# Kernel tuning notes

Measured on AMD Instinct MI355X. Metric: run time of the kernel, lower is better.

Reference implementation:

```python
import jax, jax.numpy as jnp
import numpy as np

BETA = 0.25

def setup_inputs() -> dict:
    key = jax.random.key(0)
    k1, k2 = jax.random.split(key)
    z = jax.random.normal(k1, (4096, 64, 64), dtype=jnp.float32)
    codebooks = jax.random.normal(k2, (64, 256, 64), dtype=jnp.float32)
    return {"z": z, "codebooks": codebooks}

def reference(z, codebooks):
    # z: (B, M, d); codebooks: (M, K, d)
    B, M, d = z.shape
    # squared distances (B, M, K) via ||z||^2 - 2 z.c + ||c||^2 (avoids (B,M,K,d) blowup)
    z2 = jnp.sum(z * z, axis=-1)                      # (B, M)
    c2 = jnp.sum(codebooks * codebooks, axis=-1)      # (M, K)
    zc = jnp.einsum('bmd,mkd->bmk', z, codebooks)     # (B, M, K)
    distances = z2[:, :, None] - 2.0 * zc + c2[None]  # (B, M, K)
    encoding_indices = jnp.argmin(distances, axis=-1) # (B, M) int
    # per-subspace codebook gather: codebooks[m, idx[b, m], :]
    quantized_raw = codebooks[jnp.arange(M)[None, :], encoding_indices]  # (B, M, d)
    # straight-through estimator
    quantized = z + jax.lax.stop_gradient(quantized_raw - z)
    q_loss = (BETA * jnp.mean((jax.lax.stop_gradient(quantized) - z) ** 2)
              + jnp.mean((quantized - jax.lax.stop_gradient(z)) ** 2))
    return quantized, encoding_indices, q_loss
```

## Files before the change

kernel.cpp:

```cpp
#include <hip/hip_runtime.h>

#define IDX_BASE 16777216UL
#define LOSS_IDX 17039360UL
#define EPS2 0.02f

typedef float4 f4;
typedef _Float16 half8 __attribute__((ext_vector_type(8)));
typedef float f32x4 __attribute__((ext_vector_type(4)));

__device__ __forceinline__ void gload_lds16(const float* g, float* s) {
    __builtin_amdgcn_global_load_lds(
        (const __attribute__((address_space(1))) unsigned int*)g,
        (__attribute__((address_space(3))) unsigned int*)s, 16, 0, 0);
}

__global__ __launch_bounds__(256) void pq_c2(const float* __restrict__ cb,
                                             float* __restrict__ c2) {
    int m = blockIdx.x, k = threadIdx.x;
    const f4* row = reinterpret_cast<const f4*>(cb + ((size_t)m * 256 + k) * 64);
    float s0 = 0.f, s1 = 0.f;
    #pragma unroll
    for (int i = 0; i < 16; i += 2) {
        f4 a = row[i], b = row[i + 1];
        s0 = fmaf(a.x,a.x,s0); s0 = fmaf(a.y,a.y,s0); s0 = fmaf(a.z,a.z,s0); s0 = fmaf(a.w,a.w,s0);
        s1 = fmaf(b.x,b.x,s1); s1 = fmaf(b.y,b.y,s1); s1 = fmaf(b.z,b.z,s1); s1 = fmaf(b.w,b.w,s1);
    }
    c2[m * 256 + k] = s0 + s1;
}

__global__ __launch_bounds__(256, 4) void pq_main(
    const float* __restrict__ z, const float* __restrict__ cb,
    const float* __restrict__ c2ws,
    float* __restrict__ out, float* __restrict__ partial)
{
    __shared__ f4    sZ4[128 * 16];
    __shared__ float sM1[4 * 128];
    __shared__ float sM2[4 * 128];
    __shared__ int   sK [4 * 128];
    __shared__ int   sBest[128];
    __shared__ float sW[4];

    const int tid = threadIdx.x, bx = blockIdx.x;
    const int m = bx >> 5, chunk = bx & 31;
    const int w = tid >> 6, lane = tid & 63;
    const int lh = lane >> 4, l15 = lane & 15;

    const float* __restrict__ cbm = cb + (size_t)m * (256 * 64);
    const f4* cb4m = reinterpret_cast<const f4*>(cbm);

    #pragma unroll
    for (int i = 0; i < 8; ++i) {
        int unit = i * 256 + w * 64 + lane;
        int row = unit >> 4, c4 = unit & 15;
        int c4p = c4 ^ (row & 7);
        const float* src = z + ((size_t)(chunk * 128 + row) * 64 + m) * 64 + c4p * 4;
        gload_lds16(src, (float*)&sZ4[i * 256 + w * 64]);
    }

    half8 ah[4][2], al[4][2];
    #pragma unroll
    for (int t = 0; t < 4; ++t) {
        int code = (w * 4 + t) * 16 + l15;
        const float* crow = cbm + code * 64 + lh * 8;
        #pragma unroll
        for (int s = 0; s < 2; ++s) {
            f4 a = *reinterpret_cast<const f4*>(crow + s * 32);
            f4 b = *reinterpret_cast<const f4*>(crow + s * 32 + 4);
            float v[8] = {a.x, a.y, a.z, a.w, b.x, b.y, b.z, b.w};
            #pragma unroll
            for (int e = 0; e < 8; ++e) {
                _Float16 h = (_Float16)v[e];
                ah[t][s][e] = h;
                al[t][s][e] = (_Float16)(v[e] - (float)h);
            }
        }
    }
    f32x4 c2i[4];
    #pragma unroll
    for (int t = 0; t < 4; ++t)
        #pragma unroll
        for (int r = 0; r < 4; ++r)
            c2i[t][r] = -0.5f * c2ws[m * 256 + w * 64 + t * 16 + lh * 4 + r];

    __syncthreads();

    #pragma unroll 1
    for (int rt = 0; rt < 8; ++rt) {
        const int row = rt * 16 + l15;
        const int swz = row & 7;
        const f4* zr = &sZ4[row * 16];
        const int c0 = lh << 1;
        f4 a0 = zr[(c0)     ^ swz];
        f4 a1 = zr[(c0 + 1) ^ swz];
        f4 a2 = zr[(c0 + 8) ^ swz];
        f4 a3 = zr[(c0 + 9) ^ swz];
        half8 bh0, bl0, bh1, bl1;
        {
            float v0[8] = {a0.x, a0.y, a0.z, a0.w, a1.x, a1.y, a1.z, a1.w};
            float v1[8] = {a2.x, a2.y, a2.z, a2.w, a3.x, a3.y, a3.z, a3.w};
            #pragma unroll
            for (int e = 0; e < 8; ++e) {
                _Float16 h0 = (_Float16)v0[e];
                bh0[e] = h0; bl0[e] = (_Float16)(v0[e] - (float)h0);
                _Float16 h1 = (_Float16)v1[e];
                bh1[e] = h1; bl1[e] = (_Float16)(v1[e] - (float)h1);
            }
        }
        float m1 = -1e30f, m2 = -1e30f; int k16 = 0;
        #pragma unroll
        for (int t = 0; t < 4; ++t) {
            f32x4 acc = c2i[t];
            acc = __builtin_amdgcn_mfma_f32_16x16x32_f16(ah[t][0], bh0, acc, 0, 0, 0);
            acc = __builtin_amdgcn_mfma_f32_16x16x32_f16(ah[t][1], bh1, acc, 0, 0, 0);
            acc = __builtin_amdgcn_mfma_f32_16x16x32_f16(ah[t][0], bl0, acc, 0, 0, 0);
            acc = __builtin_amdgcn_mfma_f32_16x16x32_f16(ah[t][1], bl1, acc, 0, 0, 0);
            acc = __builtin_amdgcn_mfma_f32_16x16x32_f16(al[t][0], bh0, acc, 0, 0, 0);
            acc = __builtin_amdgcn_mfma_f32_16x16x32_f16(al[t][1], bh1, acc, 0, 0, 0);
            #pragma unroll
            for (int r = 0; r < 4; ++r) {
                float v = acc[r];
                m2 = fmaxf(m2, fminf(v, m1));
                bool gt = v > m1;
                m1  = gt ? v : m1;
                k16 = gt ? (t * 16 + r) : k16;
            }
        }
        int kw = k16 + lh * 4;
        #pragma unroll
        for (int off = 16; off <= 32; off <<= 1) {
            float om1 = __shfl_xor(m1, off, 64);
            float om2 = __shfl_xor(m2, off, 64);
            int   okw = __shfl_xor(kw, off, 64);
            m2 = fmaxf(fmaxf(m2, om2), fminf(m1, om1));
            bool better = (om1 > m1) || (om1 == m1 && okw < kw);
            m1 = better ? om1 : m1;
            kw = better ? okw : kw;
        }
        if (lane < 16) {
            int r2 = rt * 16 + lane;
            sM1[w * 128 + r2] = m1;
            sM2[w * 128 + r2] = m2;
            sK [w * 128 + r2] = kw;
        }
    }
    __syncthreads();

    if (tid < 128) {
        float M1 = -1e30f, M2 = -1e30f; int K1 = 0;
        #pragma unroll
        for (int w2 = 0; w2 < 4; ++w2) {
            float v1 = sM1[w2 * 128 + tid];
            float v2 = sM2[w2 * 128 + tid];
            int   kk = w2 * 64 + sK[w2 * 128 + tid];
            M2 = fmaxf(fmaxf(M2, v2), fminf(M1, v1));
            bool better = v1 > M1;
            M1 = better ? v1 : M1;
            K1 = better ? kk : K1;
        }
        sBest[tid] = (M1 - M2 < EPS2) ? -1 : K1;
    }
    __syncthreads();

    for (int row = w; row < 128; row += 4) {
        if (sBest[row] >= 0) continue;
        int swz = row & 7;
        float bs = -1e30f; int bk = 0;
        #pragma unroll 1
        for (int j = 0; j < 4; ++j) {
            int k = j * 64 + lane;
            float s = -0.5f * c2ws[m * 256 + k];
            #pragma unroll
            for (int d4 = 0; d4 < 16; ++d4) {
                f4 c  = cb4m[k * 16 + d4];
                f4 zz = sZ4[row * 16 + (d4 ^ swz)];
                s = fmaf(zz.x, c.x, s); s = fmaf(zz.y, c.y, s);
                s = fmaf(zz.z, c.z, s); s = fmaf(zz.w, c.w, s);
            }
            if (s > bs) { bs = s; bk = k; }
        }
        #pragma unroll
        for (int off = 1; off < 64; off <<= 1) {
            float ov = __shfl_xor(bs, off, 64);
            int   ok = __shfl_xor(bk, off, 64);
            if (ov > bs || (ov == bs && ok < bk)) { bs = ov; bk = ok; }
        }
        if (lane == 0) sBest[row] = bk;
    }
    __syncthreads();

    float lsum = 0.f;
    {
        int row = tid >> 1, h = tid & 1;
        int k = sBest[row];
        int b = chunk * 128 + row;
        int swz = row & 7;
        const f4* q4 = cb4m + (size_t)k * 16 + h * 8;
        f4*       o4 = reinterpret_cast<f4*>(out + ((size_t)b * 64 + m) * 64) + h * 8;
        float l0 = 0.f, l1 = 0.f;
        #pragma unroll
        for (int c = 0; c < 8; ++c) {
            f4 qv = q4[c];
            f4 zv = sZ4[row * 16 + (((h << 3) + c) ^ swz)];
            o4[c] = qv;
            float d0 = qv.x - zv.x, d1 = qv.y - zv.y, d2 = qv.z - zv.z, d3 = qv.w - zv.w;
            l0 = fmaf(d0, d0, l0); l1 = fmaf(d1, d1, l1);
            l0 = fmaf(d2, d2, l0); l1 = fmaf(d3, d3, l1);
        }
        lsum = l0 + l1;
    }
    if (tid < 128)
        out[IDX_BASE + (size_t)(chunk * 128 + tid) * 64 + m] = (float)sBest[tid];
    #pragma unroll
    for (int off = 1; off < 64; off <<= 1) lsum += __shfl_xor(lsum, off, 64);
    if (lane == 0) sW[w] = lsum;
    __syncthreads();
    if (tid == 0) partial[bx] = (sW[0] + sW[1]) + (sW[2] + sW[3]);
}

__global__ __launch_bounds__(256) void pq_loss(const float* __restrict__ partial,
                                               float* __restrict__ out)
{
    __shared__ float sW[4];
    float s = 0.f;
    #pragma unroll
    for (int i = 0; i < 8; ++i) s += partial[threadIdx.x + i * 256];
    #pragma unroll
    for (int off = 1; off < 64; off <<= 1) s += __shfl_xor(s, off, 64);
    if ((threadIdx.x & 63) == 0) sW[threadIdx.x >> 6] = s;
    __syncthreads();
    if (threadIdx.x == 0)
        out[LOSS_IDX] = ((sW[0] + sW[1]) + (sW[2] + sW[3])) * (1.25f / 16777216.0f);
}

extern "C" void kernel_launch(void* const* d_in, const int* in_sizes, int n_in,
                              void* d_out, int out_size, void* d_ws, size_t ws_size,
                              hipStream_t stream) {
    const float* zp  = (const float*)d_in[0];
    const float* cbp = (const float*)d_in[1];
    float* outp = (float*)d_out;
    float* c2ws = (float*)d_ws;
    float* part = (float*)d_ws + 64 * 256;

    pq_c2  <<<dim3(64),   dim3(256), 0, stream>>>(cbp, c2ws);
    pq_main<<<dim3(2048), dim3(256), 0, stream>>>(zp, cbp, c2ws, outp, part);
    pq_loss<<<dim3(1),    dim3(256), 0, stream>>>(part, outp);
}
```

Baseline: 93.04 us.

## Make main kernel persistent over four 64-row chunks with double-buffered z staging

Each block now handles four 64-row chunks of one subspace instead of a single 128-row chunk, so the grid halves to 1024 blocks. The next chunk's z tile is loaded into LDS asynchronously while the current one is processed, and the codebook fragments in fp16 hi/lo form are reused across all four chunks. This amortizes the per-block codebook conversion and hides z load latency. The cost is more barriers per block and fewer blocks to fill the GPU, and smaller chunks may expose the serial fallback path more often.

```diff
diff --git a/kernel.cpp b/kernel.cpp
--- a/kernel.cpp
+++ b/kernel.cpp
@@ -3,6 +3,8 @@
 #define IDX_BASE 16777216UL
 #define LOSS_IDX 17039360UL
 #define EPS2 0.02f
+#define NCHUNK 4
+#define CROWS 64
 
 typedef float4 f4;
 typedef _Float16 half8 __attribute__((ext_vector_type(8)));
@@ -33,29 +35,33 @@
     const float* __restrict__ c2ws,
     float* __restrict__ out, float* __restrict__ partial)
 {
-    __shared__ f4    sZ4[128 * 16];
-    __shared__ float sM1[4 * 128];
-    __shared__ float sM2[4 * 128];
-    __shared__ int   sK [4 * 128];
-    __shared__ int   sBest[128];
+    __shared__ f4    sZ4[2][CROWS * 16];
+    __shared__ float sM1[4 * CROWS];
+    __shared__ float sM2[4 * CROWS];
+    __shared__ int   sK [4 * CROWS];
+    __shared__ int   sBest[CROWS];
     __shared__ float sW[4];
 
     const int tid = threadIdx.x, bx = blockIdx.x;
-    const int m = bx >> 5, chunk = bx & 31;
+    const int m = bx >> 4, g = bx & 15;
     const int w = tid >> 6, lane = tid & 63;
     const int lh = lane >> 4, l15 = lane & 15;
+    const int cbase = g * NCHUNK;
 
     const float* __restrict__ cbm = cb + (size_t)m * (256 * 64);
     const f4* cb4m = reinterpret_cast<const f4*>(cbm);
 
-    #pragma unroll
-    for (int i = 0; i < 8; ++i) {
-        int unit = i * 256 + w * 64 + lane;
-        int row = unit >> 4, c4 = unit & 15;
-        int c4p = c4 ^ (row & 7);
-        const float* src = z + ((size_t)(chunk * 128 + row) * 64 + m) * 64 + c4p * 4;
-        gload_lds16(src, (float*)&sZ4[i * 256 + w * 64]);
-    }
+    auto stage = [&](int c, int bb) {
+        #pragma unroll
+        for (int i = 0; i < 4; ++i) {
+            int unit = i * 256 + w * 64 + lane;
+            int row = unit >> 4, c4 = unit & 15;
+            int c4p = c4 ^ (row & 7);
+            const float* src = z + ((size_t)(c * 64 + row) * 64 + m) * 64 + c4p * 4;
+            gload_lds16(src, (float*)&sZ4[bb][i * 256 + w * 64]);
+        }
+    };
+    stage(cbase, 0);
 
     half8 ah[4][2], al[4][2];
     #pragma unroll
@@ -82,137 +88,145 @@
         for (int r = 0; r < 4; ++r)
             c2i[t][r] = -0.5f * c2ws[m * 256 + w * 64 + t * 16 + lh * 4 + r];
 
-    __syncthreads();
+    float lacc = 0.f;
 
     #pragma unroll 1
-    for (int rt = 0; rt < 8; ++rt) {
-        const int row = rt * 16 + l15;
-        const int swz = row & 7;
-        const f4* zr = &sZ4[row * 16];
-        const int c0 = lh << 1;
-        f4 a0 = zr[(c0)     ^ swz];
-        f4 a1 = zr[(c0 + 1) ^ swz];
-        f4 a2 = zr[(c0 + 8) ^ swz];
-        f4 a3 = zr[(c0 + 9) ^ swz];
-        half8 bh0, bl0, bh1, bl1;
+    for (int cc = 0; cc < NCHUNK; ++cc) {
+        const int cur = cc & 1, nxt = cur ^ 1;
+        const int c = cbase + cc;
+        __syncthreads();
+        if (cc + 1 < NCHUNK) stage(c + 1, nxt);
+        const f4* zt = sZ4[cur];
+
+        #pragma unroll 1
+        for (int rt = 0; rt < 4; ++rt) {
+            const int row = rt * 16 + l15;
+            const int swz = row & 7;
+            const f4* zr = &zt[row * 16];
+            const int c0 = lh << 1;
+            f4 a0 = zr[(c0)     ^ swz];
+            f4 a1 = zr[(c0 + 1) ^ swz];
+            f4 a2 = zr[(c0 + 8) ^ swz];
+            f4 a3 = zr[(c0 + 9) ^ swz];
+            half8 bh0, bl0, bh1, bl1;
+            {
+                float v0[8] = {a0.x, a0.y, a0.z, a0.w, a1.x, a1.y, a1.z, a1.w};
+                float v1[8] = {a2.x, a2.y, a2.z, a2.w, a3.x, a3.y, a3.z, a3.w};
+                #pragma unroll
+                for (int e = 0; e < 8; ++e) {
+                    _Float16 h0 = (_Float16)v0[e];
+                    bh0[e] = h0; bl0[e] = (_Float16)(v0[e] - (float)h0);
+                    _Float16 h1 = (_Float16)v1[e];
+                    bh1[e] = h1; bl1[e] = (_Float16)(v1[e] - (float)h1);
+                }
+            }
+            float m1 = -1e30f, m2 = -1e30f; int k16 = 0;
+            #pragma unroll
+            for (int t = 0; t < 4; ++t) {
+                f32x4 acc = c2i[t];
+                acc = __builtin_amdgcn_mfma_f32_16x16x32_f16(ah[t][0], bh0, acc, 0, 0, 0);
+                acc = __builtin_amdgcn_mfma_f32_16x16x32_f16(ah[t][1], bh1, acc, 0, 0, 0);
+                acc = __builtin_amdgcn_mfma_f32_16x16x32_f16(ah[t][0], bl0, acc, 0, 0, 0);
+                acc = __builtin_amdgcn_mfma_f32_16x16x32_f16(ah[t][1], bl1, acc, 0, 0, 0);
+                acc = __builtin_amdgcn_mfma_f32_16x16x32_f16(al[t][0], bh0, acc, 0, 0, 0);
+                acc = __builtin_amdgcn_mfma_f32_16x16x32_f16(al[t][1], bh1, acc, 0, 0, 0);
+                #pragma unroll
+                for (int r = 0; r < 4; ++r) {
+                    float v = acc[r];
+                    m2 = fmaxf(m2, fminf(v, m1));
+                    bool gt = v > m1;
+                    m1  = gt ? v : m1;
+                    k16 = gt ? (t * 16 + r) : k16;
+                }
+            }
+            int kw = k16 + lh * 4;
+            #pragma unroll
+            for (int off = 16; off <= 32; off <<= 1) {
+                float om1 = __shfl_xor(m1, off, 64);
+                float om2 = __shfl_xor(m2, off, 64);
+                int   okw = __shfl_xor(kw, off, 64);
+                m2 = fmaxf(fmaxf(m2, om2), fminf(m1, om1));
+                bool better = (om1 > m1) || (om1 == m1 && okw < kw);
+                m1 = better ? om1 : m1;
+                kw = better ? okw : kw;
+            }
+            if (lane < 16) {
+                int r2 = rt * 16 + lane;
+                sM1[w * CROWS + r2] = m1;
+                sM2[w * CROWS + r2] = m2;
+                sK [w * CROWS + r2] = kw;
+            }
+        }
+        __syncthreads();
+
+        if (tid < CROWS) {
+            float M1 = -1e30f, M2 = -1e30f; int K1 = 0;
+            #pragma unroll
+            for (int w2 = 0; w2 < 4; ++w2) {
+                float v1 = sM1[w2 * CROWS + tid];
+                float v2 = sM2[w2 * CROWS + tid];
+                int   kk = w2 * 64 + sK[w2 * CROWS + tid];
+                M2 = fmaxf(fmaxf(M2, v2), fminf(M1, v1));
+                bool better = v1 > M1;
+                M1 = better ? v1 : M1;
+                K1 = better ? kk : K1;
+            }
+            sBest[tid] = (M1 - M2 < EPS2) ? -1 : K1;
+        }
+        __syncthreads();
+
+        for (int row = w; row < CROWS; row += 4) {
+            if (sBest[row] >= 0) continue;
+            int swz = row & 7;
+            float bs = -1e30f; int bk = 0;
+            #pragma unroll 1
+            for (int j = 0; j < 4; ++j) {
+                int k = j * 64 + lane;
+                float s = -0.5f * c2ws[m * 256 + k];
+                #pragma unroll
+                for (int d4 = 0; d4 < 16; ++d4) {
+                    f4 cvv = cb4m[k * 16 + d4];
+                    f4 zz  = zt[row * 16 + (d4 ^ swz)];
+                    s = fmaf(zz.x, cvv.x, s); s = fmaf(zz.y, cvv.y, s);
+                    s = fmaf(zz.z, cvv.z, s); s = fmaf(zz.w, cvv.w, s);
+                }
+                if (s > bs) { bs = s; bk = k; }
+            }
+            #pragma unroll
+            for (int off = 1; off < 64; off <<= 1) {
+                float ov = __shfl_xor(bs, off, 64);
+                int   ok = __shfl_xor(bk, off, 64);
+                if (ov > bs || (ov == bs && ok < bk)) { bs = ov; bk = ok; }
+            }
+            if (lane == 0) sBest[row] = bk;
+        }
+        __syncthreads();
+
         {
-            float v0[8] = {a0.x, a0.y, a0.z, a0.w, a1.x, a1.y, a1.z, a1.w};
-            float v1[8] = {a2.x, a2.y, a2.z, a2.w, a3.x, a3.y, a3.z, a3.w};
-            #pragma unroll
-            for (int e = 0; e < 8; ++e) {
-                _Float16 h0 = (_Float16)v0[e];
-                bh0[e] = h0; bl0[e] = (_Float16)(v0[e] - (float)h0);
-                _Float16 h1 = (_Float16)v1[e];
-                bh1[e] = h1; bl1[e] = (_Float16)(v1[e] - (float)h1);
-            }
-        }
-        float m1 = -1e30f, m2 = -1e30f; int k16 = 0;
-        #pragma unroll
-        for (int t = 0; t < 4; ++t) {
-            f32x4 acc = c2i[t];
-            acc = __builtin_amdgcn_mfma_f32_16x16x32_f16(ah[t][0], bh0, acc, 0, 0, 0);
-            acc = __builtin_amdgcn_mfma_f32_16x16x32_f16(ah[t][1], bh1, acc, 0, 0, 0);
-            acc = __builtin_amdgcn_mfma_f32_16x16x32_f16(ah[t][0], bl0, acc, 0, 0, 0);
-            acc = __builtin_amdgcn_mfma_f32_16x16x32_f16(ah[t][1], bl1, acc, 0, 0, 0);
-            acc = __builtin_amdgcn_mfma_f32_16x16x32_f16(al[t][0], bh0, acc, 0, 0, 0);
-            acc = __builtin_amdgcn_mfma_f32_16x16x32_f16(al[t][1], bh1, acc, 0, 0, 0);
-            #pragma unroll
-            for (int r = 0; r < 4; ++r) {
-                float v = acc[r];
-                m2 = fmaxf(m2, fminf(v, m1));
-                bool gt = v > m1;
-                m1  = gt ? v : m1;
-                k16 = gt ? (t * 16 + r) : k16;
-            }
-        }
-        int kw = k16 + lh * 4;
-        #pragma unroll
-        for (int off = 16; off <= 32; off <<= 1) {
-            float om1 = __shfl_xor(m1, off, 64);
-            float om2 = __shfl_xor(m2, off, 64);
-            int   okw = __shfl_xor(kw, off, 64);
-            m2 = fmaxf(fmaxf(m2, om2), fminf(m1, om1));
-            bool better = (om1 > m1) || (om1 == m1 && okw < kw);
-            m1 = better ? om1 : m1;
-            kw = better ? okw : kw;
-        }
-        if (lane < 16) {
-            int r2 = rt * 16 + lane;
-            sM1[w * 128 + r2] = m1;
-            sM2[w * 128 + r2] = m2;
-            sK [w * 128 + r2] = kw;
-        }
+            int row = tid >> 2, quad = tid & 3;
+            int k = sBest[row];
+            int b = c * 64 + row;
+            int swz = row & 7;
+            const f4* q4 = cb4m + (size_t)k * 16 + quad * 4;
+            f4*       o4 = reinterpret_cast<f4*>(out + ((size_t)b * 64 + m) * 64) + quad * 4;
+            #pragma unroll
+            for (int e = 0; e < 4; ++e) {
+                f4 qv = q4[e];
+                f4 zv = zt[row * 16 + ((quad * 4 + e) ^ swz)];
+                o4[e] = qv;
+                float d0 = qv.x - zv.x, d1 = qv.y - zv.y;
+                float d2 = qv.z - zv.z, d3 = qv.w - zv.w;
+                lacc = fmaf(d0, d0, lacc); lacc = fmaf(d1, d1, lacc);
+                lacc = fmaf(d2, d2, lacc); lacc = fmaf(d3, d3, lacc);
+            }
+        }
+        if (tid < CROWS)
+            out[IDX_BASE + (size_t)(c * 64 + tid) * 64 + m] = (float)sBest[tid];
     }
-    __syncthreads();
-
-    if (tid < 128) {
-        float M1 = -1e30f, M2 = -1e30f; int K1 = 0;
-        #pragma unroll
-        for (int w2 = 0; w2 < 4; ++w2) {
-            float v1 = sM1[w2 * 128 + tid];
-            float v2 = sM2[w2 * 128 + tid];
-            int   kk = w2 * 64 + sK[w2 * 128 + tid];
-            M2 = fmaxf(fmaxf(M2, v2), fminf(M1, v1));
-            bool better = v1 > M1;
-            M1 = better ? v1 : M1;
-            K1 = better ? kk : K1;
-        }
-        sBest[tid] = (M1 - M2 < EPS2) ? -1 : K1;
-    }
-    __syncthreads();
-
-    for (int row = w; row < 128; row += 4) {
-        if (sBest[row] >= 0) continue;
-        int swz = row & 7;
-        float bs = -1e30f; int bk = 0;
-        #pragma unroll 1
-        for (int j = 0; j < 4; ++j) {
-            int k = j * 64 + lane;
-            float s = -0.5f * c2ws[m * 256 + k];
-            #pragma unroll
-            for (int d4 = 0; d4 < 16; ++d4) {
-                f4 c  = cb4m[k * 16 + d4];
-                f4 zz = sZ4[row * 16 + (d4 ^ swz)];
-                s = fmaf(zz.x, c.x, s); s = fmaf(zz.y, c.y, s);
-                s = fmaf(zz.z, c.z, s); s = fmaf(zz.w, c.w, s);
-            }
-            if (s > bs) { bs = s; bk = k; }
-        }
-        #pragma unroll
-        for (int off = 1; off < 64; off <<= 1) {
-            float ov = __shfl_xor(bs, off, 64);
-            int   ok = __shfl_xor(bk, off, 64);
-            if (ov > bs || (ov == bs && ok < bk)) { bs = ov; bk = ok; }
-        }
-        if (lane == 0) sBest[row] = bk;
-    }
-    __syncthreads();
-
-    float lsum = 0.f;
-    {
-        int row = tid >> 1, h = tid & 1;
-        int k = sBest[row];
-        int b = chunk * 128 + row;
-        int swz = row & 7;
-        const f4* q4 = cb4m + (size_t)k * 16 + h * 8;
-        f4*       o4 = reinterpret_cast<f4*>(out + ((size_t)b * 64 + m) * 64) + h * 8;
-        float l0 = 0.f, l1 = 0.f;
-        #pragma unroll
-        for (int c = 0; c < 8; ++c) {
-            f4 qv = q4[c];
-            f4 zv = sZ4[row * 16 + (((h << 3) + c) ^ swz)];
-            o4[c] = qv;
-            float d0 = qv.x - zv.x, d1 = qv.y - zv.y, d2 = qv.z - zv.z, d3 = qv.w - zv.w;
-            l0 = fmaf(d0, d0, l0); l1 = fmaf(d1, d1, l1);
-            l0 = fmaf(d2, d2, l0); l1 = fmaf(d3, d3, l1);
-        }
-        lsum = l0 + l1;
-    }
-    if (tid < 128)
-        out[IDX_BASE + (size_t)(chunk * 128 + tid) * 64 + m] = (float)sBest[tid];
-    #pragma unroll
-    for (int off = 1; off < 64; off <<= 1) lsum += __shfl_xor(lsum, off, 64);
-    if (lane == 0) sW[w] = lsum;
+
+    #pragma unroll
+    for (int off = 1; off < 64; off <<= 1) lacc += __shfl_xor(lacc, off, 64);
+    if (lane == 0) sW[w] = lacc;
     __syncthreads();
     if (tid == 0) partial[bx] = (sW[0] + sW[1]) + (sW[2] + sW[3]);
 }
@@ -221,9 +235,8 @@
                                                float* __restrict__ out)
 {
     __shared__ float sW[4];
-    float s = 0.f;
-    #pragma unroll
-    for (int i = 0; i < 8; ++i) s += partial[threadIdx.x + i * 256];
+    float s = (partial[threadIdx.x]       + partial[threadIdx.x + 256])
+            + (partial[threadIdx.x + 512] + partial[threadIdx.x + 768]);
     #pragma unroll
     for (int off = 1; off < 64; off <<= 1) s += __shfl_xor(s, off, 64);
     if ((threadIdx.x & 63) == 0) sW[threadIdx.x >> 6] = s;
@@ -242,6 +255,6 @@
     float* part = (float*)d_ws + 64 * 256;
 
     pq_c2  <<<dim3(64),   dim3(256), 0, stream>>>(cbp, c2ws);
-    pq_main<<<dim3(2048), dim3(256), 0, stream>>>(zp, cbp, c2ws, outp, part);
+    pq_main<<<dim3(1024), dim3(256), 0, stream>>>(zp, cbp, c2ws, outp, part);
     pq_loss<<<dim3(1),    dim3(256), 0, stream>>>(part, outp);
 }
```

Result: slower. 150.9 us (+62.2%).

## Swap MFMA roles: keep z fragments in registers, stream precomputed codebook fragments

Applied to the files above, without the earlier changes.

A new pre-kernel converts each subspace codebook into split fp16 hi/lo MFMA fragments once and stores them in workspace. Each wave in the main kernel now owns 32 z rows held as register fragments and loops over all 16 codebook tiles read from that buffer. This removes the LDS staging of z, the cross-wave argmin merge and most block barriers. In exchange the codebook fragments are re-read from global/L2 by every wave, and the exact-recheck path reads z straight from global memory.

```diff
diff --git a/kernel.cpp b/kernel.cpp
--- a/kernel.cpp
+++ b/kernel.cpp
@@ -7,12 +7,6 @@
 typedef float4 f4;
 typedef _Float16 half8 __attribute__((ext_vector_type(8)));
 typedef float f32x4 __attribute__((ext_vector_type(4)));
-
-__device__ __forceinline__ void gload_lds16(const float* g, float* s) {
-    __builtin_amdgcn_global_load_lds(
-        (const __attribute__((address_space(1))) unsigned int*)g,
-        (__attribute__((address_space(3))) unsigned int*)s, 16, 0, 0);
-}
 
 __global__ __launch_bounds__(256) void pq_c2(const float* __restrict__ cb,
                                              float* __restrict__ c2) {
@@ -28,193 +22,168 @@
     c2[m * 256 + k] = s0 + s1;
 }
 
-__global__ __launch_bounds__(256, 4) void pq_main(
-    const float* __restrict__ z, const float* __restrict__ cb,
-    const float* __restrict__ c2ws,
-    float* __restrict__ out, float* __restrict__ partial)
-{
-    __shared__ f4    sZ4[128 * 16];
-    __shared__ float sM1[4 * 128];
-    __shared__ float sM2[4 * 128];
-    __shared__ int   sK [4 * 128];
-    __shared__ int   sBest[128];
-    __shared__ float sW[4];
-
-    const int tid = threadIdx.x, bx = blockIdx.x;
-    const int m = bx >> 5, chunk = bx & 31;
-    const int w = tid >> 6, lane = tid & 63;
-    const int lh = lane >> 4, l15 = lane & 15;
-
-    const float* __restrict__ cbm = cb + (size_t)m * (256 * 64);
-    const f4* cb4m = reinterpret_cast<const f4*>(cbm);
-
-    #pragma unroll
-    for (int i = 0; i < 8; ++i) {
-        int unit = i * 256 + w * 64 + lane;
-        int row = unit >> 4, c4 = unit & 15;
-        int c4p = c4 ^ (row & 7);
-        const float* src = z + ((size_t)(chunk * 128 + row) * 64 + m) * 64 + c4p * 4;
-        gload_lds16(src, (float*)&sZ4[i * 256 + w * 64]);
-    }
-
-    half8 ah[4][2], al[4][2];
-    #pragma unroll
-    for (int t = 0; t < 4; ++t) {
-        int code = (w * 4 + t) * 16 + l15;
+__global__ __launch_bounds__(256) void pq_frag(const float* __restrict__ cb,
+                                               half8* __restrict__ fragbuf) {
+    int m = blockIdx.x, tid = threadIdx.x;
+    int w = tid >> 6, lane = tid & 63, lh = lane >> 4, l15 = lane & 15;
+    const float* cbm = cb + (size_t)m * (256 * 64);
+    half8* fbm = fragbuf + (size_t)m * (16 * 4 * 64);
+    #pragma unroll
+    for (int ti = 0; ti < 4; ++ti) {
+        int tile = w * 4 + ti;
+        int code = tile * 16 + l15;
         const float* crow = cbm + code * 64 + lh * 8;
         #pragma unroll
         for (int s = 0; s < 2; ++s) {
             f4 a = *reinterpret_cast<const f4*>(crow + s * 32);
             f4 b = *reinterpret_cast<const f4*>(crow + s * 32 + 4);
             float v[8] = {a.x, a.y, a.z, a.w, b.x, b.y, b.z, b.w};
+            half8 hi, lo;
             #pragma unroll
             for (int e = 0; e < 8; ++e) {
                 _Float16 h = (_Float16)v[e];
-                ah[t][s][e] = h;
-                al[t][s][e] = (_Float16)(v[e] - (float)h);
-            }
-        }
-    }
-    f32x4 c2i[4];
-    #pragma unroll
-    for (int t = 0; t < 4; ++t)
-        #pragma unroll
-        for (int r = 0; r < 4; ++r)
-            c2i[t][r] = -0.5f * c2ws[m * 256 + w * 64 + t * 16 + lh * 4 + r];
-
-    __syncthreads();
-
-    #pragma unroll 1
-    for (int rt = 0; rt < 8; ++rt) {
-        const int row = rt * 16 + l15;
-        const int swz = row & 7;
-        const f4* zr = &sZ4[row * 16];
-        const int c0 = lh << 1;
-        f4 a0 = zr[(c0)     ^ swz];
-        f4 a1 = zr[(c0 + 1) ^ swz];
-        f4 a2 = zr[(c0 + 8) ^ swz];
-        f4 a3 = zr[(c0 + 9) ^ swz];
-        half8 bh0, bl0, bh1, bl1;
-        {
-            float v0[8] = {a0.x, a0.y, a0.z, a0.w, a1.x, a1.y, a1.z, a1.w};
-            float v1[8] = {a2.x, a2.y, a2.z, a2.w, a3.x, a3.y, a3.z, a3.w};
-            #pragma unroll
-            for (int e = 0; e < 8; ++e) {
-                _Float16 h0 = (_Float16)v0[e];
-                bh0[e] = h0; bl0[e] = (_Float16)(v0[e] - (float)h0);
-                _Float16 h1 = (_Float16)v1[e];
-                bh1[e] = h1; bl1[e] = (_Float16)(v1[e] - (float)h1);
-            }
-        }
-        float m1 = -1e30f, m2 = -1e30f; int k16 = 0;
-        #pragma unroll
-        for (int t = 0; t < 4; ++t) {
-            f32x4 acc = c2i[t];
-            acc = __builtin_amdgcn_mfma_f32_16x16x32_f16(ah[t][0], bh0, acc, 0, 0, 0);
-            acc = __builtin_amdgcn_mfma_f32_16x16x32_f16(ah[t][1], bh1, acc, 0, 0, 0);
-            acc = __builtin_amdgcn_mfma_f32_16x16x32_f16(ah[t][0], bl0, acc, 0, 0, 0);
-            acc = __builtin_amdgcn_mfma_f32_16x16x32_f16(ah[t][1], bl1, acc, 0, 0, 0);
-            acc = __builtin_amdgcn_mfma_f32_16x16x32_f16(al[t][0], bh0, acc, 0, 0, 0);
-            acc = __builtin_amdgcn_mfma_f32_16x16x32_f16(al[t][1], bh1, acc, 0, 0, 0);
+                hi[e] = h; lo[e] = (_Float16)(v[e] - (float)h);
+            }
+            fbm[(tile * 4 + s * 2 + 0) * 64 + lane] = hi;
+            fbm[(tile * 4 + s * 2 + 1) * 64 + lane] = lo;
+        }
+    }
+}
+
+__global__ __launch_bounds__(256, 4) void pq_main(
+    const float* __restrict__ z, const float* __restrict__ cb,
+    const float* __restrict__ c2ws, const half8* __restrict__ fragbuf,
+    float* __restrict__ out, float* __restrict__ partial)
+{
+    const int tid = threadIdx.x, bx = blockIdx.x;
+    const int m = bx >> 5;
+    const int w = tid >> 6, lane = tid & 63;
+    const int lh = lane >> 4, l15 = lane & 15;
+    const int rowbase = (bx & 31) * 128 + w * 32;
+
+    const float* __restrict__ cbm = cb + (size_t)m * (256 * 64);
+    const f4* cb4m = reinterpret_cast<const f4*>(cbm);
+    const half8* __restrict__ fb = fragbuf + (size_t)m * (16 * 4 * 64);
+    const f4* __restrict__ c2t = reinterpret_cast<const f4*>(c2ws + m * 256);
+
+    half8 zh0[2], zl0[2], zh1[2], zl1[2];
+    #pragma unroll
+    for (int h = 0; h < 2; ++h) {
+        size_t rh = (size_t)(rowbase + h * 16 + l15);
+        const float* zb = z + (rh * 64 + m) * 64 + lh * 8;
+        f4 p0 = *reinterpret_cast<const f4*>(zb);
+        f4 p1 = *reinterpret_cast<const f4*>(zb + 4);
+        f4 p2 = *reinterpret_cast<const f4*>(zb + 32);
+        f4 p3 = *reinterpret_cast<const f4*>(zb + 36);
+        float v0[8] = {p0.x,p0.y,p0.z,p0.w,p1.x,p1.y,p1.z,p1.w};
+        float v1[8] = {p2.x,p2.y,p2.z,p2.w,p3.x,p3.y,p3.z,p3.w};
+        #pragma unroll
+        for (int e = 0; e < 8; ++e) {
+            _Float16 a = (_Float16)v0[e];
+            zh0[h][e] = a; zl0[h][e] = (_Float16)(v0[e] - (float)a);
+            _Float16 b = (_Float16)v1[e];
+            zh1[h][e] = b; zl1[h][e] = (_Float16)(v1[e] - (float)b);
+        }
+    }
+
+    float m1[2] = {-1e30f, -1e30f}, m2[2] = {-1e30f, -1e30f};
+    int   bk[2] = {0, 0};
+
+    #pragma unroll 4
+    for (int tile = 0; tile < 16; ++tile) {
+        half8 ah0 = fb[(tile * 4 + 0) * 64 + lane];
+        half8 al0 = fb[(tile * 4 + 1) * 64 + lane];
+        half8 ah1 = fb[(tile * 4 + 2) * 64 + lane];
+        half8 al1 = fb[(tile * 4 + 3) * 64 + lane];
+        f4 cv = c2t[tile * 4 + lh];
+        f32x4 ci; ci[0] = -0.5f*cv.x; ci[1] = -0.5f*cv.y; ci[2] = -0.5f*cv.z; ci[3] = -0.5f*cv.w;
+        #pragma unroll
+        for (int h = 0; h < 2; ++h) {
+            f32x4 acc = ci;
+            acc = __builtin_amdgcn_mfma_f32_16x16x32_f16(ah0, h ? zh0[1] : zh0[0], acc, 0, 0, 0);
+            acc = __builtin_amdgcn_mfma_f32_16x16x32_f16(ah1, h ? zh1[1] : zh1[0], acc, 0, 0, 0);
+            acc = __builtin_amdgcn_mfma_f32_16x16x32_f16(ah0, h ? zl0[1] : zl0[0], acc, 0, 0, 0);
+            acc = __builtin_amdgcn_mfma_f32_16x16x32_f16(ah1, h ? zl1[1] : zl1[0], acc, 0, 0, 0);
+            acc = __builtin_amdgcn_mfma_f32_16x16x32_f16(al0, h ? zh0[1] : zh0[0], acc, 0, 0, 0);
+            acc = __builtin_amdgcn_mfma_f32_16x16x32_f16(al1, h ? zh1[1] : zh1[0], acc, 0, 0, 0);
             #pragma unroll
             for (int r = 0; r < 4; ++r) {
                 float v = acc[r];
-                m2 = fmaxf(m2, fminf(v, m1));
-                bool gt = v > m1;
-                m1  = gt ? v : m1;
-                k16 = gt ? (t * 16 + r) : k16;
-            }
-        }
-        int kw = k16 + lh * 4;
+                int code = tile * 16 + lh * 4 + r;
+                m2[h] = fmaxf(m2[h], fminf(v, m1[h]));
+                bool gt = v > m1[h];
+                m1[h] = gt ? v : m1[h];
+                bk[h] = gt ? code : bk[h];
+            }
+        }
+    }
+
+    float lsum = 0.f;
+    #pragma unroll
+    for (int h = 0; h < 2; ++h) {
         #pragma unroll
         for (int off = 16; off <= 32; off <<= 1) {
-            float om1 = __shfl_xor(m1, off, 64);
-            float om2 = __shfl_xor(m2, off, 64);
-            int   okw = __shfl_xor(kw, off, 64);
-            m2 = fmaxf(fmaxf(m2, om2), fminf(m1, om1));
-            bool better = (om1 > m1) || (om1 == m1 && okw < kw);
-            m1 = better ? om1 : m1;
-            kw = better ? okw : kw;
-        }
-        if (lane < 16) {
-            int r2 = rt * 16 + lane;
-            sM1[w * 128 + r2] = m1;
-            sM2[w * 128 + r2] = m2;
-            sK [w * 128 + r2] = kw;
-        }
-    }
-    __syncthreads();
-
-    if (tid < 128) {
-        float M1 = -1e30f, M2 = -1e30f; int K1 = 0;
-        #pragma unroll
-        for (int w2 = 0; w2 < 4; ++w2) {
-            float v1 = sM1[w2 * 128 + tid];
-            float v2 = sM2[w2 * 128 + tid];
-            int   kk = w2 * 64 + sK[w2 * 128 + tid];
-            M2 = fmaxf(fmaxf(M2, v2), fminf(M1, v1));
-            bool better = v1 > M1;
-            M1 = better ? v1 : M1;
-            K1 = better ? kk : K1;
-        }
-        sBest[tid] = (M1 - M2 < EPS2) ? -1 : K1;
-    }
-    __syncthreads();
-
-    for (int row = w; row < 128; row += 4) {
-        if (sBest[row] >= 0) continue;
-        int swz = row & 7;
-        float bs = -1e30f; int bk = 0;
-        #pragma unroll 1
-        for (int j = 0; j < 4; ++j) {
-            int k = j * 64 + lane;
-            float s = -0.5f * c2ws[m * 256 + k];
+            float om1 = __shfl_xor(m1[h], off, 64);
+            float om2 = __shfl_xor(m2[h], off, 64);
+            int   obk = __shfl_xor(bk[h], off, 64);
+            m2[h] = fmaxf(fmaxf(m2[h], om2), fminf(m1[h], om1));
+            bool better = (om1 > m1[h]) || (om1 == m1[h] && obk < bk[h]);
+            m1[h] = better ? om1 : m1[h];
+            bk[h] = better ? obk : bk[h];
+        }
+        bool need = (m1[h] - m2[h] < EPS2);
+        unsigned mask = (unsigned)(__ballot(need)) & 0xFFFFu;
+        while (mask) {
+            int row = __builtin_ctz(mask); mask &= mask - 1;
+            size_t rg = (size_t)(rowbase + h * 16 + row);
+            const f4* zr4 = reinterpret_cast<const f4*>(z + (rg * 64 + m) * 64);
+            float bs = -1e30f; int bkx = 0;
+            #pragma unroll 1
+            for (int j = 0; j < 4; ++j) {
+                int k = j * 64 + lane;
+                float s = -0.5f * c2ws[m * 256 + k];
+                #pragma unroll
+                for (int d4 = 0; d4 < 16; ++d4) {
+                    f4 c = cb4m[k * 16 + d4];
+                    f4 zz = zr4[d4];
+                    s = fmaf(zz.x, c.x, s); s = fmaf(zz.y, c.y, s);
+                    s = fmaf(zz.z, c.z, s); s = fmaf(zz.w, c.w, s);
+                }
+                if (s > bs) { bs = s; bkx = k; }
+            }
             #pragma unroll
-            for (int d4 = 0; d4 < 16; ++d4) {
-                f4 c  = cb4m[k * 16 + d4];
-                f4 zz = sZ4[row * 16 + (d4 ^ swz)];
-                s = fmaf(zz.x, c.x, s); s = fmaf(zz.y, c.y, s);
-                s = fmaf(zz.z, c.z, s); s = fmaf(zz.w, c.w, s);
-            }
-            if (s > bs) { bs = s; bk = k; }
-        }
-        #pragma unroll
-        for (int off = 1; off < 64; off <<= 1) {
-            float ov = __shfl_xor(bs, off, 64);
-            int   ok = __shfl_xor(bk, off, 64);
-            if (ov > bs || (ov == bs && ok < bk)) { bs = ov; bk = ok; }
-        }
-        if (lane == 0) sBest[row] = bk;
-    }
-    __syncthreads();
-
-    float lsum = 0.f;
-    {
-        int row = tid >> 1, h = tid & 1;
-        int k = sBest[row];
-        int b = chunk * 128 + row;
-        int swz = row & 7;
-        const f4* q4 = cb4m + (size_t)k * 16 + h * 8;
-        f4*       o4 = reinterpret_cast<f4*>(out + ((size_t)b * 64 + m) * 64) + h * 8;
-        float l0 = 0.f, l1 = 0.f;
-        #pragma unroll
-        for (int c = 0; c < 8; ++c) {
-            f4 qv = q4[c];
-            f4 zv = sZ4[row * 16 + (((h << 3) + c) ^ swz)];
-            o4[c] = qv;
-            float d0 = qv.x - zv.x, d1 = qv.y - zv.y, d2 = qv.z - zv.z, d3 = qv.w - zv.w;
-            l0 = fmaf(d0, d0, l0); l1 = fmaf(d1, d1, l1);
-            l0 = fmaf(d2, d2, l0); l1 = fmaf(d3, d3, l1);
-        }
-        lsum = l0 + l1;
-    }
-    if (tid < 128)
-        out[IDX_BASE + (size_t)(chunk * 128 + tid) * 64 + m] = (float)sBest[tid];
+            for (int off = 1; off < 64; off <<= 1) {
+                float ov = __shfl_xor(bs, off, 64);
+                int   ok = __shfl_xor(bkx, off, 64);
+                if (ov > bs || (ov == bs && ok < bkx)) { bs = ov; bkx = ok; }
+            }
+            bk[h] = (l15 == row) ? bkx : bk[h];
+        }
+        size_t rg = (size_t)(rowbase + h * 16 + l15);
+        int k = bk[h];
+        const f4* qb = reinterpret_cast<const f4*>(cbm + (size_t)k * 64 + lh * 8);
+        f4 q0 = qb[0], q1 = qb[1], q2 = qb[8], q3 = qb[9];
+        float* ob = out + (rg * 64 + m) * 64 + lh * 8;
+        *reinterpret_cast<f4*>(ob)      = q0;
+        *reinterpret_cast<f4*>(ob + 4)  = q1;
+        *reinterpret_cast<f4*>(ob + 32) = q2;
+        *reinterpret_cast<f4*>(ob + 36) = q3;
+        float qq0[8] = {q0.x,q0.y,q0.z,q0.w,q1.x,q1.y,q1.z,q1.w};
+        float qq1[8] = {q2.x,q2.y,q2.z,q2.w,q3.x,q3.y,q3.z,q3.w};
+        #pragma unroll
+        for (int e = 0; e < 8; ++e) {
+            float zr0 = (float)(h ? zh0[1][e] : zh0[0][e]) + (float)(h ? zl0[1][e] : zl0[0][e]);
+            float zr1 = (float)(h ? zh1[1][e] : zh1[0][e]) + (float)(h ? zl1[1][e] : zl1[0][e]);
+            float d0 = qq0[e] - zr0, d1 = qq1[e] - zr1;
+            lsum = fmaf(d0, d0, lsum); lsum = fmaf(d1, d1, lsum);
+        }
+        if (lane < 16)
+            out[IDX_BASE + rg * 64 + m] = (float)bk[h];
+    }
+
     #pragma unroll
     for (int off = 1; off < 64; off <<= 1) lsum += __shfl_xor(lsum, off, 64);
-    if (lane == 0) sW[w] = lsum;
-    __syncthreads();
-    if (tid == 0) partial[bx] = (sW[0] + sW[1]) + (sW[2] + sW[3]);
+    if (lane == 0) partial[bx * 4 + w] = lsum;
 }
 
 __global__ __launch_bounds__(256) void pq_loss(const float* __restrict__ partial,
@@ -223,7 +192,7 @@
     __shared__ float sW[4];
     float s = 0.f;
     #pragma unroll
-    for (int i = 0; i < 8; ++i) s += partial[threadIdx.x + i * 256];
+    for (int i = 0; i < 32; ++i) s += partial[threadIdx.x + i * 256];
     #pragma unroll
     for (int off = 1; off < 64; off <<= 1) s += __shfl_xor(s, off, 64);
     if ((threadIdx.x & 63) == 0) sW[threadIdx.x >> 6] = s;
@@ -239,9 +208,11 @@
     const float* cbp = (const float*)d_in[1];
     float* outp = (float*)d_out;
     float* c2ws = (float*)d_ws;
-    float* part = (float*)d_ws + 64 * 256;
+    half8* frag = (half8*)((float*)d_ws + 16384);
+    float* part = (float*)d_ws + 16384 + 1048576;
 
     pq_c2  <<<dim3(64),   dim3(256), 0, stream>>>(cbp, c2ws);
-    pq_main<<<dim3(2048), dim3(256), 0, stream>>>(zp, cbp, c2ws, outp, part);
+    pq_frag<<<dim3(64),   dim3(256), 0, stream>>>(cbp, frag);
+    pq_main<<<dim3(2048), dim3(256), 0, stream>>>(zp, cbp, c2ws, frag, outp, part);
     pq_loss<<<dim3(1),    dim3(256), 0, stream>>>(part, outp);
 }
```

Result: slower. 113.8 us (+22.3%).

## Precompute split-fp16 codebook fragments, remap block order, process two row tiles per iteration

Applied to the files above, without the earlier changes.

A new pre-pass kernel converts each codebook into hi/lo fp16 MFMA fragments once and stores them in the workspace, so each of the 2048 main blocks loads ready fragments instead of reconverting 64 KB of fp32 codebook. Block-to-(m,chunk) mapping is changed so that consecutive blocks cover different subspaces, c2 is loaded as float4, and the row-tile loop now handles two 16-row tiles per iteration with med3 for the runner-up tracking, exposing more independent MFMA chains. Launch bounds occupancy is lowered from 4 to 3 to accommodate the extra registers, and an additional kernel launch is added.

```diff
diff --git a/kernel.cpp b/kernel.cpp
--- a/kernel.cpp
+++ b/kernel.cpp
@@ -28,9 +28,37 @@
     c2[m * 256 + k] = s0 + s1;
 }
 
-__global__ __launch_bounds__(256, 4) void pq_main(
+__global__ __launch_bounds__(256) void pq_frag(const float* __restrict__ cb,
+                                               half8* __restrict__ fragbuf) {
+    int m = blockIdx.x, tid = threadIdx.x;
+    int w = tid >> 6, lane = tid & 63, lh = lane >> 4, l15 = lane & 15;
+    const float* cbm = cb + (size_t)m * (256 * 64);
+    half8* fbm = fragbuf + (size_t)m * (16 * 4 * 64);
+    #pragma unroll
+    for (int ti = 0; ti < 4; ++ti) {
+        int tile = w * 4 + ti;
+        int code = tile * 16 + l15;
+        const float* crow = cbm + code * 64 + lh * 8;
+        #pragma unroll
+        for (int s = 0; s < 2; ++s) {
+            f4 a = *reinterpret_cast<const f4*>(crow + s * 32);
+            f4 b = *reinterpret_cast<const f4*>(crow + s * 32 + 4);
+            float v[8] = {a.x, a.y, a.z, a.w, b.x, b.y, b.z, b.w};
+            half8 hi, lo;
+            #pragma unroll
+            for (int e = 0; e < 8; ++e) {
+                _Float16 h = (_Float16)v[e];
+                hi[e] = h; lo[e] = (_Float16)(v[e] - (float)h);
+            }
+            fbm[(tile * 4 + s * 2 + 0) * 64 + lane] = hi;
+            fbm[(tile * 4 + s * 2 + 1) * 64 + lane] = lo;
+        }
+    }
+}
+
+__global__ __launch_bounds__(256, 3) void pq_main(
     const float* __restrict__ z, const float* __restrict__ cb,
-    const float* __restrict__ c2ws,
+    const float* __restrict__ c2ws, const half8* __restrict__ fragbuf,
     float* __restrict__ out, float* __restrict__ partial)
 {
     __shared__ f4    sZ4[128 * 16];
@@ -41,7 +69,8 @@
     __shared__ float sW[4];
 
     const int tid = threadIdx.x, bx = blockIdx.x;
-    const int m = bx >> 5, chunk = bx & 31;
+    const int m = ((bx & 7) << 3) | ((bx >> 3) & 7);
+    const int chunk = bx >> 6;
     const int w = tid >> 6, lane = tid & 63;
     const int lh = lane >> 4, l15 = lane & 15;
 
@@ -57,90 +86,93 @@
         gload_lds16(src, (float*)&sZ4[i * 256 + w * 64]);
     }
 
+    const half8* __restrict__ fb = fragbuf + (size_t)m * (16 * 4 * 64);
     half8 ah[4][2], al[4][2];
     #pragma unroll
     for (int t = 0; t < 4; ++t) {
-        int code = (w * 4 + t) * 16 + l15;
-        const float* crow = cbm + code * 64 + lh * 8;
         #pragma unroll
         for (int s = 0; s < 2; ++s) {
-            f4 a = *reinterpret_cast<const f4*>(crow + s * 32);
-            f4 b = *reinterpret_cast<const f4*>(crow + s * 32 + 4);
-            float v[8] = {a.x, a.y, a.z, a.w, b.x, b.y, b.z, b.w};
-            #pragma unroll
-            for (int e = 0; e < 8; ++e) {
-                _Float16 h = (_Float16)v[e];
-                ah[t][s][e] = h;
-                al[t][s][e] = (_Float16)(v[e] - (float)h);
-            }
-        }
-    }
+            ah[t][s] = fb[((w * 4 + t) * 4 + s * 2 + 0) * 64 + lane];
+            al[t][s] = fb[((w * 4 + t) * 4 + s * 2 + 1) * 64 + lane];
+        }
+    }
+    const f4* __restrict__ c2t = reinterpret_cast<const f4*>(c2ws + m * 256);
     f32x4 c2i[4];
     #pragma unroll
-    for (int t = 0; t < 4; ++t)
-        #pragma unroll
-        for (int r = 0; r < 4; ++r)
-            c2i[t][r] = -0.5f * c2ws[m * 256 + w * 64 + t * 16 + lh * 4 + r];
+    for (int t = 0; t < 4; ++t) {
+        f4 cv = c2t[(w * 4 + t) * 4 + lh];
+        c2i[t][0] = -0.5f*cv.x; c2i[t][1] = -0.5f*cv.y;
+        c2i[t][2] = -0.5f*cv.z; c2i[t][3] = -0.5f*cv.w;
+    }
 
     __syncthreads();
 
     #pragma unroll 1
-    for (int rt = 0; rt < 8; ++rt) {
-        const int row = rt * 16 + l15;
-        const int swz = row & 7;
-        const f4* zr = &sZ4[row * 16];
-        const int c0 = lh << 1;
-        f4 a0 = zr[(c0)     ^ swz];
-        f4 a1 = zr[(c0 + 1) ^ swz];
-        f4 a2 = zr[(c0 + 8) ^ swz];
-        f4 a3 = zr[(c0 + 9) ^ swz];
-        half8 bh0, bl0, bh1, bl1;
-        {
-            float v0[8] = {a0.x, a0.y, a0.z, a0.w, a1.x, a1.y, a1.z, a1.w};
-            float v1[8] = {a2.x, a2.y, a2.z, a2.w, a3.x, a3.y, a3.z, a3.w};
+    for (int rtp = 0; rtp < 4; ++rtp) {
+        half8 bh0[2], bl0[2], bh1[2], bl1[2];
+        #pragma unroll
+        for (int h = 0; h < 2; ++h) {
+            const int row = (rtp * 2 + h) * 16 + l15;
+            const int swz = row & 7;
+            const f4* zr = &sZ4[row * 16];
+            const int c0 = lh << 1;
+            f4 a0 = zr[(c0)     ^ swz];
+            f4 a1 = zr[(c0 + 1) ^ swz];
+            f4 a2 = zr[(c0 + 8) ^ swz];
+            f4 a3 = zr[(c0 + 9) ^ swz];
+            float v0[8] = {a0.x,a0.y,a0.z,a0.w,a1.x,a1.y,a1.z,a1.w};
+            float v1[8] = {a2.x,a2.y,a2.z,a2.w,a3.x,a3.y,a3.z,a3.w};
             #pragma unroll
             for (int e = 0; e < 8; ++e) {
                 _Float16 h0 = (_Float16)v0[e];
-                bh0[e] = h0; bl0[e] = (_Float16)(v0[e] - (float)h0);
+                bh0[h][e] = h0; bl0[h][e] = (_Float16)(v0[e] - (float)h0);
                 _Float16 h1 = (_Float16)v1[e];
-                bh1[e] = h1; bl1[e] = (_Float16)(v1[e] - (float)h1);
-            }
-        }
-        float m1 = -1e30f, m2 = -1e30f; int k16 = 0;
+                bh1[h][e] = h1; bl1[h][e] = (_Float16)(v1[e] - (float)h1);
+            }
+        }
+        float m1[2] = {-1e30f, -1e30f}, m2[2] = {-1e30f, -1e30f};
+        int k16[2] = {0, 0};
         #pragma unroll
         for (int t = 0; t < 4; ++t) {
-            f32x4 acc = c2i[t];
-            acc = __builtin_amdgcn_mfma_f32_16x16x32_f16(ah[t][0], bh0, acc, 0, 0, 0);
-            acc = __builtin_amdgcn_mfma_f32_16x16x32_f16(ah[t][1], bh1, acc, 0, 0, 0);
-            acc = __builtin_amdgcn_mfma_f32_16x16x32_f16(ah[t][0], bl0, acc, 0, 0, 0);
-            acc = __builtin_amdgcn_mfma_f32_16x16x32_f16(ah[t][1], bl1, acc, 0, 0, 0);
-            acc = __builtin_amdgcn_mfma_f32_16x16x32_f16(al[t][0], bh0, acc, 0, 0, 0);
-            acc = __builtin_amdgcn_mfma_f32_16x16x32_f16(al[t][1], bh1, acc, 0, 0, 0);
-            #pragma unroll
-            for (int r = 0; r < 4; ++r) {
-                float v = acc[r];
-                m2 = fmaxf(m2, fminf(v, m1));
-                bool gt = v > m1;
-                m1  = gt ? v : m1;
-                k16 = gt ? (t * 16 + r) : k16;
-            }
-        }
-        int kw = k16 + lh * 4;
-        #pragma unroll
-        for (int off = 16; off <= 32; off <<= 1) {
-            float om1 = __shfl_xor(m1, off, 64);
-            float om2 = __shfl_xor(m2, off, 64);
-            int   okw = __shfl_xor(kw, off, 64);
-            m2 = fmaxf(fmaxf(m2, om2), fminf(m1, om1));
-            bool better = (om1 > m1) || (om1 == m1 && okw < kw);
-            m1 = better ? om1 : m1;
-            kw = better ? okw : kw;
-        }
-        if (lane < 16) {
-            int r2 = rt * 16 + lane;
-            sM1[w * 128 + r2] = m1;
-            sM2[w * 128 + r2] = m2;
-            sK [w * 128 + r2] = kw;
+            #pragma unroll
+            for (int h = 0; h < 2; ++h) {
+                f32x4 acc = c2i[t];
+                acc = __builtin_amdgcn_mfma_f32_16x16x32_f16(ah[t][0], bh0[h], acc, 0, 0, 0);
+                acc = __builtin_amdgcn_mfma_f32_16x16x32_f16(ah[t][1], bh1[h], acc, 0, 0, 0);
+                acc = __builtin_amdgcn_mfma_f32_16x16x32_f16(ah[t][0], bl0[h], acc, 0, 0, 0);
+                acc = __builtin_amdgcn_mfma_f32_16x16x32_f16(ah[t][1], bl1[h], acc, 0, 0, 0);
+                acc = __builtin_amdgcn_mfma_f32_16x16x32_f16(al[t][0], bh0[h], acc, 0, 0, 0);
+                acc = __builtin_amdgcn_mfma_f32_16x16x32_f16(al[t][1], bh1[h], acc, 0, 0, 0);
+                #pragma unroll
+                for (int r = 0; r < 4; ++r) {
+                    float v = acc[r];
+                    m2[h] = __builtin_amdgcn_fmed3f(v, m1[h], m2[h]);
+                    bool gt = v > m1[h];
+                    m1[h]  = gt ? v : m1[h];
+                    k16[h] = gt ? (t * 16 + r) : k16[h];
+                }
+            }
+        }
+        #pragma unroll
+        for (int h = 0; h < 2; ++h) {
+            int kw = k16[h] + lh * 4;
+            float a1v = m1[h], a2v = m2[h];
+            #pragma unroll
+            for (int off = 16; off <= 32; off <<= 1) {
+                float om1 = __shfl_xor(a1v, off, 64);
+                float om2 = __shfl_xor(a2v, off, 64);
+                int   okw = __shfl_xor(kw, off, 64);
+                a2v = fmaxf(fmaxf(a2v, om2), fminf(a1v, om1));
+                bool better = (om1 > a1v) || (om1 == a1v && okw < kw);
+                a1v = better ? om1 : a1v;
+                kw  = better ? okw : kw;
+            }
+            if (lane < 16) {
+                int r2 = (rtp * 2 + h) * 16 + lane;
+                sM1[w * 128 + r2] = a1v;
+                sM2[w * 128 + r2] = a2v;
+                sK [w * 128 + r2] = kw;
+            }
         }
     }
     __syncthreads();
@@ -171,10 +203,10 @@
             float s = -0.5f * c2ws[m * 256 + k];
             #pragma unroll
             for (int d4 = 0; d4 < 16; ++d4) {
-                f4 c  = cb4m[k * 16 + d4];
-                f4 zz = sZ4[row * 16 + (d4 ^ swz)];
-                s = fmaf(zz.x, c.x, s); s = fmaf(zz.y, c.y, s);
-                s = fmaf(zz.z, c.z, s); s = fmaf(zz.w, c.w, s);
+                f4 cvv = cb4m[k * 16 + d4];
+                f4 zz  = sZ4[row * 16 + (d4 ^ swz)];
+                s = fmaf(zz.x, cvv.x, s); s = fmaf(zz.y, cvv.y, s);
+                s = fmaf(zz.z, cvv.z, s); s = fmaf(zz.w, cvv.w, s);
             }
             if (s > bs) { bs = s; bk = k; }
         }
@@ -239,9 +271,11 @@
     const float* cbp = (const float*)d_in[1];
     float* outp = (float*)d_out;
     float* c2ws = (float*)d_ws;
-    float* part = (float*)d_ws + 64 * 256;
+    half8* frag = (half8*)((float*)d_ws + 16384);
+    float* part = (float*)d_ws + 16384 + 1048576;
 
     pq_c2  <<<dim3(64),   dim3(256), 0, stream>>>(cbp, c2ws);
-    pq_main<<<dim3(2048), dim3(256), 0, stream>>>(zp, cbp, c2ws, outp, part);
+    pq_frag<<<dim3(64),   dim3(256), 0, stream>>>(cbp, frag);
+    pq_main<<<dim3(2048), dim3(256), 0, stream>>>(zp, cbp, c2ws, frag, outp, part);
     pq_loss<<<dim3(1),    dim3(256), 0, stream>>>(part, outp);
 }
```

Result: faster. 89.40 us (-3.9%).
